# Optimization experiments

Hardware: AMD Instinct MI355X
Metric: run time of the kernel (lower is better)

## Reference

```python
import jax, jax.numpy as jnp
import numpy as np

EPS = 1e-5
QMAX = 127.0

def activation_quant(x):
    # per-token (last-dim) abs-max int8 fake-quant
    x_max = jnp.clip(jnp.max(jnp.abs(x), axis=-1, keepdims=True), EPS, None)
    scale = QMAX / x_max
    q = jnp.clip(jnp.round(x * scale), -128.0, 127.0)
    return q / scale

def setup_inputs() -> dict:
    key = jax.random.key(0)
    kx, kw = jax.random.split(key)
    x = jax.random.normal(kx, (4, 8192, 2048), dtype=jnp.float32)
    # ternary {-1, 0, 1} weight, stored int8 in torch, cast to float for the GEMM
    W = jax.random.randint(kw, (2048, 2048), -1, 2).astype(jnp.float32)  # [out, in]
    return {"x": x, "W": W}

def reference(x, W):
    # straight-through estimator form: x + sg(quant(x) - x)
    x_quant = x + jax.lax.stop_gradient(activation_quant(x) - x)
    # y = x_quant @ W.T  (F.linear)
    return jnp.einsum('bsd,od->bso', x_quant, W)
```

## Files before the change

### kernel.cpp

```cpp
#include <hip/hip_runtime.h>

typedef int v4i __attribute__((ext_vector_type(4)));

#define KDIM 2048
#define NDIM 2048

#define GLOAD16(g, l) __builtin_amdgcn_global_load_lds(                      \
    (const __attribute__((address_space(1))) void*)(g),                      \
    (__attribute__((address_space(3))) void*)(l), 16, 0, 0)


__device__ __forceinline__ int pack4q(float4 v, float s) {
  int a = __float2int_rn(v.x * s);
  int b = __float2int_rn(v.y * s);
  int c = __float2int_rn(v.z * s);
  int d = __float2int_rn(v.w * s);
  a = max(-128, min(127, a)); b = max(-128, min(127, b));
  c = max(-128, min(127, c)); d = max(-128, min(127, d));
  return (a & 0xff) | ((b & 0xff) << 8) | ((c & 0xff) << 16) | ((d & 0xff) << 24);
}

__global__ __launch_bounds__(256) void quant_rows(const float* __restrict__ x,
                                                  signed char* __restrict__ q,
                                                  float* __restrict__ rscale) {
  const int row = blockIdx.x;
  const float4* xr = (const float4*)(x + (size_t)row * KDIM);
  float4 v0 = xr[threadIdx.x];
  float4 v1 = xr[256 + threadIdx.x];
  float m = fmaxf(fmaxf(fabsf(v0.x), fabsf(v0.y)), fmaxf(fabsf(v0.z), fabsf(v0.w)));
  m = fmaxf(m, fmaxf(fmaxf(fabsf(v1.x), fabsf(v1.y)), fmaxf(fabsf(v1.z), fabsf(v1.w))));
  #pragma unroll
  for (int off = 32; off > 0; off >>= 1) m = fmaxf(m, __shfl_xor(m, off));
  __shared__ float red[4];
  if ((threadIdx.x & 63) == 0) red[threadIdx.x >> 6] = m;
  __syncthreads();
  float xmax = fmaxf(fmaxf(red[0], red[1]), fmaxf(red[2], red[3]));
  xmax = fmaxf(xmax, 1e-5f);
  const float scale = 127.0f / xmax;
  int* qr = (int*)(q + (size_t)row * KDIM);
  qr[threadIdx.x] = pack4q(v0, scale);
  qr[256 + threadIdx.x] = pack4q(v1, scale);
  if (threadIdx.x == 0) rscale[row] = xmax * (1.0f / 127.0f);
}

__global__ __launch_bounds__(256) void quant_w(const float* __restrict__ W,
                                               signed char* __restrict__ Wq) {
  const int i = blockIdx.x * 256 + threadIdx.x;
  float4 v = ((const float4*)W)[i];
  int a = (int)v.x, b = (int)v.y, c = (int)v.z, d = (int)v.w;
  ((int*)Wq)[i] = (a & 0xff) | ((b & 0xff) << 8) | ((c & 0xff) << 16) | ((d & 0xff) << 24);
}


#define VM6 asm volatile("s_waitcnt vmcnt(6)" ::: "memory")
#define VM0 asm volatile("s_waitcnt vmcnt(0)" ::: "memory")
#define VMNONE

#define STAGE(U, T)                                                          \
  GLOAD16(sa + (T) * 64,             lds + (U) * 24576 + dstw);              \
  GLOAD16(sa + (T) * 64 + 64 * KDIM, lds + (U) * 24576 + 4096 + dstw);       \
  GLOAD16(sb + (T) * 64,             lds + (U) * 24576 + 8192 + dstw);       \
  GLOAD16(sb + (T) * 64 + 64 * KDIM, lds + (U) * 24576 + 12288 + dstw);      \
  GLOAD16(sb + (T) * 64 + 128 * KDIM, lds + (U) * 24576 + 16384 + dstw);     \
  GLOAD16(sb + (T) * 64 + 192 * KDIM, lds + (U) * 24576 + 20480 + dstw);

#define MF1(m, n, A, BF) acc[m][n] = __builtin_amdgcn_mfma_i32_16x16x64_i8((A), (BF), acc[m][n], 0, 0, 0);

#define KTILE(U, T, DOSTAGE, VMEND)                                          \
  {                                                                          \
    if (DOSTAGE) { STAGE((((U) + 2) % 3), (T) + 2) }                         \
    v4i b0 = *(const v4i*)(lds + (U) * 24576 + bRd);                         \
    v4i b1 = *(const v4i*)(lds + (U) * 24576 + bRd + 1024);                  \
    v4i b2 = *(const v4i*)(lds + (U) * 24576 + bRd + 2048);                  \
    v4i b3 = *(const v4i*)(lds + (U) * 24576 + bRd + 3072);                  \
    v4i b4 = *(const v4i*)(lds + (U) * 24576 + bRd + 4096);                  \
    v4i b5 = *(const v4i*)(lds + (U) * 24576 + bRd + 5120);                  \
    v4i b6 = *(const v4i*)(lds + (U) * 24576 + bRd + 6144);                  \
    v4i b7 = *(const v4i*)(lds + (U) * 24576 + bRd + 7168);                  \
    v4i a0 = *(const v4i*)(lds + (U) * 24576 + aRd);                         \
    v4i a1 = *(const v4i*)(lds + (U) * 24576 + aRd + 1024);                  \
    v4i a2 = *(const v4i*)(lds + (U) * 24576 + aRd + 2048);                  \
    v4i a3 = *(const v4i*)(lds + (U) * 24576 + aRd + 3072);                  \
    __builtin_amdgcn_s_setprio(1);                                           \
    MF1(0, 0, a0, b0) MF1(0, 1, a0, b1) MF1(0, 2, a0, b2) MF1(0, 3, a0, b3)  \
    MF1(0, 4, a0, b4) MF1(0, 5, a0, b5) MF1(0, 6, a0, b6) MF1(0, 7, a0, b7)  \
    MF1(1, 0, a1, b0) MF1(1, 1, a1, b1) MF1(1, 2, a1, b2) MF1(1, 3, a1, b3)  \
    MF1(1, 4, a1, b4) MF1(1, 5, a1, b5) MF1(1, 6, a1, b6) MF1(1, 7, a1, b7)  \
    MF1(2, 0, a2, b0) MF1(2, 1, a2, b1) MF1(2, 2, a2, b2) MF1(2, 3, a2, b3)  \
    MF1(2, 4, a2, b4) MF1(2, 5, a2, b5) MF1(2, 6, a2, b6) MF1(2, 7, a2, b7)  \
    MF1(3, 0, a3, b0) MF1(3, 1, a3, b1) MF1(3, 2, a3, b2) MF1(3, 3, a3, b3)  \
    MF1(3, 4, a3, b4) MF1(3, 5, a3, b5) MF1(3, 6, a3, b6) MF1(3, 7, a3, b7)  \
    __builtin_amdgcn_s_setprio(0);                                           \
    VMEND;                                                                   \
    __builtin_amdgcn_s_barrier();                                            \
    __builtin_amdgcn_sched_barrier(0);                                       \
  }

__global__ __launch_bounds__(256, 2) void gemm_i8(const signed char* __restrict__ A,
                                                  const signed char* __restrict__ B,
                                                  const float* __restrict__ rscale,
                                                  float* __restrict__ C) {
  __shared__ __align__(16) signed char lds[3 * 24576];
  const int bid = blockIdx.x;
  const int lid = (bid & 7) * 256 + (bid >> 3);
  const int bm = lid >> 3;
  const int bn = lid & 7;
  const int tid = threadIdx.x;
  const int wid = tid >> 6;
  const int lane = tid & 63;
  const int wr = wid >> 1, wc = wid & 1;

  const int srow = wid * 16 + (lane >> 2);
  const int scol = (((lane & 3) ^ ((lane >> 3) & 3)) << 4);
  const signed char* sa = A + (size_t)(bm * 128 + srow) * KDIM + scol;
  const signed char* sb = B + (size_t)(bn * 256 + srow) * KDIM + scol;
  const int dstw = wid << 10;

  const int rslot = (((lane >> 4) ^ ((lane >> 1) & 3)) << 4);
  const int aRd = (wr * 64 + (lane & 15)) * 64 + rslot;
  const int bRd = 8192 + (wc * 128 + (lane & 15)) * 64 + rslot;

  v4i acc[4][8] = {};

  STAGE(0, 0)
  STAGE(1, 1)
  VM6;
  __builtin_amdgcn_s_barrier();
  __builtin_amdgcn_sched_barrier(0);

  for (int ti = 0; ti < 10; ++ti) {
    const int t = ti * 3;
    KTILE(0, t + 0, 1, VM6)
    KTILE(1, t + 1, 1, VM6)
    KTILE(2, t + 2, 1, VM6)
  }
  KTILE(0, 30, 0, VM0)
  KTILE(1, 31, 0, VMNONE)

  const int col0 = bn * 256 + wc * 128 + (lane & 15);
  const int rbase = bm * 128 + wr * 64 + ((lane >> 4) << 2);
  #pragma unroll
  for (int m = 0; m < 4; ++m) {
    #pragma unroll
    for (int r = 0; r < 4; ++r) {
      const int row = rbase + m * 16 + r;
      const float s = rscale[row];
      float* crow = C + (size_t)row * NDIM + col0;
      #pragma unroll
      for (int n = 0; n < 8; ++n) crow[n * 16] = (float)acc[m][n][r] * s;
    }
  }
}

extern "C" void kernel_launch(void* const* d_in, const int* in_sizes, int n_in,
                              void* d_out, int out_size, void* d_ws, size_t ws_size,
                              hipStream_t stream) {
  const float* x = (const float*)d_in[0];
  const float* W = (const float*)d_in[1];
  float* out = (float*)d_out;
  const int M = in_sizes[0] / KDIM;

  signed char* q = (signed char*)d_ws;
  signed char* Wq = q + (size_t)M * KDIM;
  float* rscale = (float*)(Wq + (size_t)NDIM * KDIM);

  quant_rows<<<M, 256, 0, stream>>>(x, q, rscale);
  quant_w<<<(NDIM * KDIM / 4) / 256, 256, 0, stream>>>(W, Wq);
  gemm_i8<<<(M / 128) * (NDIM / 256), 256, 0, stream>>>(q, Wq, rscale, out);
}
```

Measured before the change: 238.1 us.

## Load int8 A fragments directly from global into registers, stage only B in LDS

The activation (A) tile no longer goes through LDS. Each wave now reads its MFMA A fragments straight from global memory into a double-buffered register set, prefetched one k-tile ahead, while B keeps the 3-stage LDS pipeline. This cuts LDS capacity and LDS read traffic per block and shortens the vmcnt window. In exchange, A latency is hidden only one tile ahead, the two waves sharing the same A rows both load them (more L2 traffic), and the per-lane 16-byte row-strided loads may coalesce less well.

```diff
diff --git a/kernel.cpp b/kernel.cpp
--- a/kernel.cpp
+++ b/kernel.cpp
@@ -52,44 +52,44 @@
 }
 
 
-#define VM6 asm volatile("s_waitcnt vmcnt(6)" ::: "memory")
+#define VM4 asm volatile("s_waitcnt vmcnt(4)" ::: "memory")
 #define VM0 asm volatile("s_waitcnt vmcnt(0)" ::: "memory")
 #define VMNONE
 
-#define STAGE(U, T)                                                          \
-  GLOAD16(sa + (T) * 64,             lds + (U) * 24576 + dstw);              \
-  GLOAD16(sa + (T) * 64 + 64 * KDIM, lds + (U) * 24576 + 4096 + dstw);       \
-  GLOAD16(sb + (T) * 64,             lds + (U) * 24576 + 8192 + dstw);       \
-  GLOAD16(sb + (T) * 64 + 64 * KDIM, lds + (U) * 24576 + 12288 + dstw);      \
-  GLOAD16(sb + (T) * 64 + 128 * KDIM, lds + (U) * 24576 + 16384 + dstw);     \
-  GLOAD16(sb + (T) * 64 + 192 * KDIM, lds + (U) * 24576 + 20480 + dstw);
+#define STAGE_B(U, T)                                                        \
+  GLOAD16(sb + (T) * 64,              lds + (U) * 16384 + dstw);             \
+  GLOAD16(sb + (T) * 64 +  64 * KDIM, lds + (U) * 16384 + 4096 + dstw);     \
+  GLOAD16(sb + (T) * 64 + 128 * KDIM, lds + (U) * 16384 + 8192 + dstw);     \
+  GLOAD16(sb + (T) * 64 + 192 * KDIM, lds + (U) * 16384 + 12288 + dstw);
 
 #define MF1(m, n, A, BF) acc[m][n] = __builtin_amdgcn_mfma_i32_16x16x64_i8((A), (BF), acc[m][n], 0, 0, 0);
 
-#define KTILE(U, T, DOSTAGE, VMEND)                                          \
+#define KTILE(U, T, CA, NA, DOREAD, DOSTAGE, VMEND)                          \
   {                                                                          \
-    if (DOSTAGE) { STAGE((((U) + 2) % 3), (T) + 2) }                         \
-    v4i b0 = *(const v4i*)(lds + (U) * 24576 + bRd);                         \
-    v4i b1 = *(const v4i*)(lds + (U) * 24576 + bRd + 1024);                  \
-    v4i b2 = *(const v4i*)(lds + (U) * 24576 + bRd + 2048);                  \
-    v4i b3 = *(const v4i*)(lds + (U) * 24576 + bRd + 3072);                  \
-    v4i b4 = *(const v4i*)(lds + (U) * 24576 + bRd + 4096);                  \
-    v4i b5 = *(const v4i*)(lds + (U) * 24576 + bRd + 5120);                  \
-    v4i b6 = *(const v4i*)(lds + (U) * 24576 + bRd + 6144);                  \
-    v4i b7 = *(const v4i*)(lds + (U) * 24576 + bRd + 7168);                  \
-    v4i a0 = *(const v4i*)(lds + (U) * 24576 + aRd);                         \
-    v4i a1 = *(const v4i*)(lds + (U) * 24576 + aRd + 1024);                  \
-    v4i a2 = *(const v4i*)(lds + (U) * 24576 + aRd + 2048);                  \
-    v4i a3 = *(const v4i*)(lds + (U) * 24576 + aRd + 3072);                  \
+    if (DOREAD) {                                                            \
+      NA##0 = *(const v4i*)(pa0 + ((T) + 1) * 64);                           \
+      NA##1 = *(const v4i*)(pa1 + ((T) + 1) * 64);                           \
+      NA##2 = *(const v4i*)(pa2 + ((T) + 1) * 64);                           \
+      NA##3 = *(const v4i*)(pa3 + ((T) + 1) * 64);                           \
+    }                                                                        \
+    if (DOSTAGE) { STAGE_B((((U) + 2) % 3), (T) + 2) }                       \
+    v4i b0 = *(const v4i*)(lds + (U) * 16384 + bRd);                         \
+    v4i b1 = *(const v4i*)(lds + (U) * 16384 + bRd + 1024);                  \
+    v4i b2 = *(const v4i*)(lds + (U) * 16384 + bRd + 2048);                  \
+    v4i b3 = *(const v4i*)(lds + (U) * 16384 + bRd + 3072);                  \
+    v4i b4 = *(const v4i*)(lds + (U) * 16384 + bRd + 4096);                  \
+    v4i b5 = *(const v4i*)(lds + (U) * 16384 + bRd + 5120);                  \
+    v4i b6 = *(const v4i*)(lds + (U) * 16384 + bRd + 6144);                  \
+    v4i b7 = *(const v4i*)(lds + (U) * 16384 + bRd + 7168);                  \
     __builtin_amdgcn_s_setprio(1);                                           \
-    MF1(0, 0, a0, b0) MF1(0, 1, a0, b1) MF1(0, 2, a0, b2) MF1(0, 3, a0, b3)  \
-    MF1(0, 4, a0, b4) MF1(0, 5, a0, b5) MF1(0, 6, a0, b6) MF1(0, 7, a0, b7)  \
-    MF1(1, 0, a1, b0) MF1(1, 1, a1, b1) MF1(1, 2, a1, b2) MF1(1, 3, a1, b3)  \
-    MF1(1, 4, a1, b4) MF1(1, 5, a1, b5) MF1(1, 6, a1, b6) MF1(1, 7, a1, b7)  \
-    MF1(2, 0, a2, b0) MF1(2, 1, a2, b1) MF1(2, 2, a2, b2) MF1(2, 3, a2, b3)  \
-    MF1(2, 4, a2, b4) MF1(2, 5, a2, b5) MF1(2, 6, a2, b6) MF1(2, 7, a2, b7)  \
-    MF1(3, 0, a3, b0) MF1(3, 1, a3, b1) MF1(3, 2, a3, b2) MF1(3, 3, a3, b3)  \
-    MF1(3, 4, a3, b4) MF1(3, 5, a3, b5) MF1(3, 6, a3, b6) MF1(3, 7, a3, b7)  \
+    MF1(0, 0, CA##0, b0) MF1(0, 1, CA##0, b1) MF1(0, 2, CA##0, b2) MF1(0, 3, CA##0, b3) \
+    MF1(0, 4, CA##0, b4) MF1(0, 5, CA##0, b5) MF1(0, 6, CA##0, b6) MF1(0, 7, CA##0, b7) \
+    MF1(1, 0, CA##1, b0) MF1(1, 1, CA##1, b1) MF1(1, 2, CA##1, b2) MF1(1, 3, CA##1, b3) \
+    MF1(1, 4, CA##1, b4) MF1(1, 5, CA##1, b5) MF1(1, 6, CA##1, b6) MF1(1, 7, CA##1, b7) \
+    MF1(2, 0, CA##2, b0) MF1(2, 1, CA##2, b1) MF1(2, 2, CA##2, b2) MF1(2, 3, CA##2, b3) \
+    MF1(2, 4, CA##2, b4) MF1(2, 5, CA##2, b5) MF1(2, 6, CA##2, b6) MF1(2, 7, CA##2, b7) \
+    MF1(3, 0, CA##3, b0) MF1(3, 1, CA##3, b1) MF1(3, 2, CA##3, b2) MF1(3, 3, CA##3, b3) \
+    MF1(3, 4, CA##3, b4) MF1(3, 5, CA##3, b5) MF1(3, 6, CA##3, b6) MF1(3, 7, CA##3, b7) \
     __builtin_amdgcn_s_setprio(0);                                           \
     VMEND;                                                                   \
     __builtin_amdgcn_s_barrier();                                            \
@@ -100,7 +100,7 @@
                                                   const signed char* __restrict__ B,
                                                   const float* __restrict__ rscale,
                                                   float* __restrict__ C) {
-  __shared__ __align__(16) signed char lds[3 * 24576];
+  __shared__ __align__(16) signed char lds[3 * 16384];
   const int bid = blockIdx.x;
   const int lid = (bid & 7) * 256 + (bid >> 3);
   const int bm = lid >> 3;
@@ -112,30 +112,42 @@
 
   const int srow = wid * 16 + (lane >> 2);
   const int scol = (((lane & 3) ^ ((lane >> 3) & 3)) << 4);
-  const signed char* sa = A + (size_t)(bm * 128 + srow) * KDIM + scol;
   const signed char* sb = B + (size_t)(bn * 256 + srow) * KDIM + scol;
   const int dstw = wid << 10;
 
   const int rslot = (((lane >> 4) ^ ((lane >> 1) & 3)) << 4);
-  const int aRd = (wr * 64 + (lane & 15)) * 64 + rslot;
-  const int bRd = 8192 + (wc * 128 + (lane & 15)) * 64 + rslot;
+  const int bRd = (wc * 128 + (lane & 15)) * 64 + rslot;
+
+  const size_t abase = (size_t)(bm * 128 + wr * 64 + (lane & 15)) * KDIM + ((lane >> 4) << 4);
+  const signed char* pa0 = A + abase;
+  const signed char* pa1 = A + abase + (size_t)16 * KDIM;
+  const signed char* pa2 = A + abase + (size_t)32 * KDIM;
+  const signed char* pa3 = A + abase + (size_t)48 * KDIM;
 
   v4i acc[4][8] = {};
+  v4i fX0, fX1, fX2, fX3, fY0, fY1, fY2, fY3;
 
-  STAGE(0, 0)
-  STAGE(1, 1)
-  VM6;
+  fX0 = *(const v4i*)(pa0);
+  fX1 = *(const v4i*)(pa1);
+  fX2 = *(const v4i*)(pa2);
+  fX3 = *(const v4i*)(pa3);
+  STAGE_B(0, 0)
+  STAGE_B(1, 1)
+  VM4;
   __builtin_amdgcn_s_barrier();
   __builtin_amdgcn_sched_barrier(0);
 
-  for (int ti = 0; ti < 10; ++ti) {
-    const int t = ti * 3;
-    KTILE(0, t + 0, 1, VM6)
-    KTILE(1, t + 1, 1, VM6)
-    KTILE(2, t + 2, 1, VM6)
+  for (int ti = 0; ti < 5; ++ti) {
+    const int t = ti * 6;
+    KTILE(0, t + 0, fX, fY, 1, 1, VM4)
+    KTILE(1, t + 1, fY, fX, 1, 1, VM4)
+    KTILE(2, t + 2, fX, fY, 1, 1, VM4)
+    KTILE(0, t + 3, fY, fX, 1, 1, VM4)
+    KTILE(1, t + 4, fX, fY, 1, 1, VM4)
+    KTILE(2, t + 5, fY, fX, 1, 1, VM4)
   }
-  KTILE(0, 30, 0, VM0)
-  KTILE(1, 31, 0, VMNONE)
+  KTILE(0, 30, fX, fY, 1, 0, VM0)
+  KTILE(1, 31, fY, fX, 0, 0, VMNONE)
 
   const int col0 = bn * 256 + wc * 128 + (lane & 15);
   const int rbase = bm * 128 + wr * 64 + ((lane >> 4) << 2);
```

Measured after the change: 304.4 us. +27.8%, slower.

## Shrink GEMM tile to 128x128 with double-buffered LDS and higher occupancy

Applied to the files above, without the earlier changes.

Reduces the int8 GEMM block tile from 128x256 to 128x128, changes the LDS pipeline from three-stage with partial vmcnt waits to two-stage double buffering issued after the MFMAs with full vmcnt(0) waits, and raises launch bounds to three blocks per CU. The block-index swizzle is adjusted for the doubled grid. The aim is to rely on occupancy rather than deep in-block prefetch to hide latency. The trade-off is lower per-block data reuse (more A reloads), a stricter wait each k-tile, and reduced software pipelining depth.

```diff
diff --git a/kernel.cpp b/kernel.cpp
--- a/kernel.cpp
+++ b/kernel.cpp
@@ -48,63 +48,50 @@
   const int i = blockIdx.x * 256 + threadIdx.x;
   float4 v = ((const float4*)W)[i];
   int a = (int)v.x, b = (int)v.y, c = (int)v.z, d = (int)v.w;
-  ((int*)Wq)[i] = (a & 0xff) | ((b & 0xff) << 8) | ((c & 0xff) << 16) | ((d & 0xff) << 24);
+  ((int*)Wq)[i] = (a & 0xff) | ((b << 8) & 0xff00) | ((c << 16) & 0xff0000) | (d << 24);
 }
 
 
-#define VM6 asm volatile("s_waitcnt vmcnt(6)" ::: "memory")
 #define VM0 asm volatile("s_waitcnt vmcnt(0)" ::: "memory")
-#define VMNONE
 
 #define STAGE(U, T)                                                          \
-  GLOAD16(sa + (T) * 64,             lds + (U) * 24576 + dstw);              \
-  GLOAD16(sa + (T) * 64 + 64 * KDIM, lds + (U) * 24576 + 4096 + dstw);       \
-  GLOAD16(sb + (T) * 64,             lds + (U) * 24576 + 8192 + dstw);       \
-  GLOAD16(sb + (T) * 64 + 64 * KDIM, lds + (U) * 24576 + 12288 + dstw);      \
-  GLOAD16(sb + (T) * 64 + 128 * KDIM, lds + (U) * 24576 + 16384 + dstw);     \
-  GLOAD16(sb + (T) * 64 + 192 * KDIM, lds + (U) * 24576 + 20480 + dstw);
+  GLOAD16(sa + (T) * 64,            lds + (U) * 16384 + dstw);               \
+  GLOAD16(sa + (T) * 64 + 64 * KDIM, lds + (U) * 16384 + 4096 + dstw);       \
+  GLOAD16(sb + (T) * 64,            lds + (U) * 16384 + 8192 + dstw);        \
+  GLOAD16(sb + (T) * 64 + 64 * KDIM, lds + (U) * 16384 + 12288 + dstw);
 
 #define MF1(m, n, A, BF) acc[m][n] = __builtin_amdgcn_mfma_i32_16x16x64_i8((A), (BF), acc[m][n], 0, 0, 0);
 
-#define KTILE(U, T, DOSTAGE, VMEND)                                          \
+#define KTILE(U, T, DOSTAGE)                                                 \
   {                                                                          \
-    if (DOSTAGE) { STAGE((((U) + 2) % 3), (T) + 2) }                         \
-    v4i b0 = *(const v4i*)(lds + (U) * 24576 + bRd);                         \
-    v4i b1 = *(const v4i*)(lds + (U) * 24576 + bRd + 1024);                  \
-    v4i b2 = *(const v4i*)(lds + (U) * 24576 + bRd + 2048);                  \
-    v4i b3 = *(const v4i*)(lds + (U) * 24576 + bRd + 3072);                  \
-    v4i b4 = *(const v4i*)(lds + (U) * 24576 + bRd + 4096);                  \
-    v4i b5 = *(const v4i*)(lds + (U) * 24576 + bRd + 5120);                  \
-    v4i b6 = *(const v4i*)(lds + (U) * 24576 + bRd + 6144);                  \
-    v4i b7 = *(const v4i*)(lds + (U) * 24576 + bRd + 7168);                  \
-    v4i a0 = *(const v4i*)(lds + (U) * 24576 + aRd);                         \
-    v4i a1 = *(const v4i*)(lds + (U) * 24576 + aRd + 1024);                  \
-    v4i a2 = *(const v4i*)(lds + (U) * 24576 + aRd + 2048);                  \
-    v4i a3 = *(const v4i*)(lds + (U) * 24576 + aRd + 3072);                  \
+    v4i a0 = *(const v4i*)(lds + (U) * 16384 + aRd);                         \
+    v4i a1 = *(const v4i*)(lds + (U) * 16384 + aRd + 1024);                  \
+    v4i a2 = *(const v4i*)(lds + (U) * 16384 + aRd + 2048);                  \
+    v4i a3 = *(const v4i*)(lds + (U) * 16384 + aRd + 3072);                  \
+    v4i b0 = *(const v4i*)(lds + (U) * 16384 + bRd);                         \
+    v4i b1 = *(const v4i*)(lds + (U) * 16384 + bRd + 1024);                  \
+    v4i b2 = *(const v4i*)(lds + (U) * 16384 + bRd + 2048);                  \
+    v4i b3 = *(const v4i*)(lds + (U) * 16384 + bRd + 3072);                  \
     __builtin_amdgcn_s_setprio(1);                                           \
     MF1(0, 0, a0, b0) MF1(0, 1, a0, b1) MF1(0, 2, a0, b2) MF1(0, 3, a0, b3)  \
-    MF1(0, 4, a0, b4) MF1(0, 5, a0, b5) MF1(0, 6, a0, b6) MF1(0, 7, a0, b7)  \
     MF1(1, 0, a1, b0) MF1(1, 1, a1, b1) MF1(1, 2, a1, b2) MF1(1, 3, a1, b3)  \
-    MF1(1, 4, a1, b4) MF1(1, 5, a1, b5) MF1(1, 6, a1, b6) MF1(1, 7, a1, b7)  \
     MF1(2, 0, a2, b0) MF1(2, 1, a2, b1) MF1(2, 2, a2, b2) MF1(2, 3, a2, b3)  \
-    MF1(2, 4, a2, b4) MF1(2, 5, a2, b5) MF1(2, 6, a2, b6) MF1(2, 7, a2, b7)  \
     MF1(3, 0, a3, b0) MF1(3, 1, a3, b1) MF1(3, 2, a3, b2) MF1(3, 3, a3, b3)  \
-    MF1(3, 4, a3, b4) MF1(3, 5, a3, b5) MF1(3, 6, a3, b6) MF1(3, 7, a3, b7)  \
     __builtin_amdgcn_s_setprio(0);                                           \
-    VMEND;                                                                   \
+    if (DOSTAGE) { STAGE((U) ^ 1, (T) + 1) }                                 \
+    VM0;                                                                     \
     __builtin_amdgcn_s_barrier();                                            \
-    __builtin_amdgcn_sched_barrier(0);                                       \
   }
 
-__global__ __launch_bounds__(256, 2) void gemm_i8(const signed char* __restrict__ A,
+__global__ __launch_bounds__(256, 3) void gemm_i8(const signed char* __restrict__ A,
                                                   const signed char* __restrict__ B,
                                                   const float* __restrict__ rscale,
                                                   float* __restrict__ C) {
-  __shared__ __align__(16) signed char lds[3 * 24576];
+  __shared__ __align__(16) signed char lds[32768];
   const int bid = blockIdx.x;
-  const int lid = (bid & 7) * 256 + (bid >> 3);
-  const int bm = lid >> 3;
-  const int bn = lid & 7;
+  const int lid = (bid & 7) * 512 + (bid >> 3);
+  const int bm = lid >> 4;
+  const int bn = lid & 15;
   const int tid = threadIdx.x;
   const int wid = tid >> 6;
   const int lane = tid & 63;
@@ -113,31 +100,27 @@
   const int srow = wid * 16 + (lane >> 2);
   const int scol = (((lane & 3) ^ ((lane >> 3) & 3)) << 4);
   const signed char* sa = A + (size_t)(bm * 128 + srow) * KDIM + scol;
-  const signed char* sb = B + (size_t)(bn * 256 + srow) * KDIM + scol;
+  const signed char* sb = B + (size_t)(bn * 128 + srow) * KDIM + scol;
   const int dstw = wid << 10;
 
   const int rslot = (((lane >> 4) ^ ((lane >> 1) & 3)) << 4);
   const int aRd = (wr * 64 + (lane & 15)) * 64 + rslot;
-  const int bRd = 8192 + (wc * 128 + (lane & 15)) * 64 + rslot;
+  const int bRd = 8192 + (wc * 64 + (lane & 15)) * 64 + rslot;
 
-  v4i acc[4][8] = {};
+  v4i acc[4][4] = {};
 
   STAGE(0, 0)
-  STAGE(1, 1)
-  VM6;
+  VM0;
   __builtin_amdgcn_s_barrier();
-  __builtin_amdgcn_sched_barrier(0);
 
-  for (int ti = 0; ti < 10; ++ti) {
-    const int t = ti * 3;
-    KTILE(0, t + 0, 1, VM6)
-    KTILE(1, t + 1, 1, VM6)
-    KTILE(2, t + 2, 1, VM6)
+  for (int ti = 0; ti < 15; ++ti) {
+    KTILE(0, 2 * ti + 0, 1)
+    KTILE(1, 2 * ti + 1, 1)
   }
-  KTILE(0, 30, 0, VM0)
-  KTILE(1, 31, 0, VMNONE)
+  KTILE(0, 30, 1)
+  KTILE(1, 31, 0)
 
-  const int col0 = bn * 256 + wc * 128 + (lane & 15);
+  const int col0 = bn * 128 + wc * 64 + (lane & 15);
   const int rbase = bm * 128 + wr * 64 + ((lane >> 4) << 2);
   #pragma unroll
   for (int m = 0; m < 4; ++m) {
@@ -147,7 +130,7 @@
       const float s = rscale[row];
       float* crow = C + (size_t)row * NDIM + col0;
       #pragma unroll
-      for (int n = 0; n < 8; ++n) crow[n * 16] = (float)acc[m][n][r] * s;
+      for (int n = 0; n < 4; ++n) crow[n * 16] = (float)acc[m][n][r] * s;
     }
   }
 }
@@ -166,5 +149,5 @@
 
   quant_rows<<<M, 256, 0, stream>>>(x, q, rscale);
   quant_w<<<(NDIM * KDIM / 4) / 256, 256, 0, stream>>>(W, Wq);
-  gemm_i8<<<(M / 128) * (NDIM / 256), 256, 0, stream>>>(q, Wq, rscale, out);
+  gemm_i8<<<(M / 128) * (NDIM / 128), 256, 0, stream>>>(q, Wq, rscale, out);
 }
```

After: 276.7 us. 16.2% more time.
